# Optimization experiments

Measured on AMD Instinct MI355X. Metric: run time of the kernel, lower is better.

## Reference

```python
import jax, jax.numpy as jnp
import numpy as np

N_NODES = 50000
N_EDGES = 800000
IN_CH = 64
HID = 64
HID2 = HID // 2  # 32


def _sage_conv(x, src, dst, w_l, w_r, b, n_nodes):
    """PyG SAGEConv (aggr='mean', root_weight=True):
    out = lin_l(mean_{j in N(i)} x_j) + lin_r(x_i), bias in lin_l.
    Messages flow src -> dst (source_to_target)."""
    msg = x[src]  # [E, d] gather of source features
    summed = jax.ops.segment_sum(msg, dst, num_segments=n_nodes)  # [N, d]
    cnt = jax.ops.segment_sum(jnp.ones((src.shape[0],), x.dtype), dst,
                              num_segments=n_nodes)  # [N]
    mean = summed / jnp.maximum(cnt, 1.0)[:, None]
    return mean @ w_l + b + x @ w_r


def setup_inputs() -> dict:
    key = jax.random.key(0)
    ks = jax.random.split(key, 12)
    s = 0.05
    x = jax.random.normal(ks[0], (N_NODES, IN_CH), dtype=jnp.float32)
    edge_index = jax.random.randint(ks[1], (2, N_EDGES), 0, N_NODES, dtype=jnp.int32)
    return {
        "x": x,
        "edge_index": edge_index,
        # SAGEConv layer 1 (in -> hidden)
        "w1_l": jax.random.normal(ks[2], (IN_CH, HID), dtype=jnp.float32) * s,
        "w1_r": jax.random.normal(ks[3], (IN_CH, HID), dtype=jnp.float32) * s,
        "b1": jnp.zeros((HID,), jnp.float32),
        # SAGEConv layer 2 (hidden -> hidden//2)
        "w2_l": jax.random.normal(ks[4], (HID, HID2), dtype=jnp.float32) * s,
        "w2_r": jax.random.normal(ks[5], (HID, HID2), dtype=jnp.float32) * s,
        "b2": jnp.zeros((HID2,), jnp.float32),
        # classifier MLP: Linear(32,16) -> ReLU -> Linear(16,2)
        "wc1": jax.random.normal(ks[6], (HID2, 16), dtype=jnp.float32) * s,
        "bc1": jnp.zeros((16,), jnp.float32),
        "wc2": jax.random.normal(ks[7], (16, 2), dtype=jnp.float32) * s,
        "bc2": jnp.zeros((2,), jnp.float32),
    }


def reference(x, edge_index, w1_l, w1_r, b1, w2_l, w2_r, b2, wc1, bc1, wc2, bc2):
    src, dst = edge_index[0], edge_index[1]
    n = x.shape[0]
    # Dropout is identity in eval / deterministic reference.
    h = jax.nn.relu(_sage_conv(x, src, dst, w1_l, w1_r, b1, n))
    h = jax.nn.relu(_sage_conv(h, src, dst, w2_l, w2_r, b2, n))
    h = jax.nn.relu(h @ wc1 + bc1)
    out = h @ wc2 + bc2  # [N, 2]
    return out
```

## Files before the change

kernel.cpp:

```cpp
#include <hip/hip_runtime.h>
#include <hip/hip_fp16.h>

#define N_NODES 50000
#define N_EDGES 800000
#define NBINS   391
#define CAP     4096
#define EPB     4096
#define NBLK_E  ((N_EDGES + EPB - 1) / EPB)
#define NTILE   391
#define LSTRIDE 129

__global__ __launch_bounds__(512) void k_binA_pre1(
        const int* __restrict__ src, const int* __restrict__ dst,
        int* __restrict__ bincur, int* __restrict__ binned,
        const float* __restrict__ x,
        const float* __restrict__ wl, const float* __restrict__ wr,
        const float* __restrict__ b,
        __half* __restrict__ ph, float* __restrict__ q) {
    __shared__ float smem[64 * LSTRIDE];
    int t = threadIdx.x;
    int bb = blockIdx.x;
    if (bb < NBLK_E) {
        int* cnt  = (int*)smem;
        int* sc   = cnt + 392;
        int* lpos = sc + 512;
        int* base = lpos + 392;
        int* stage = base + 392;
        unsigned short* sbin = (unsigned short*)(stage + EPB);
        int blkbase = bb * EPB;
        int nE = min(EPB, N_EDGES - blkbase);
        for (int i = t; i < NBINS; i += 512) cnt[i] = 0;
        __syncthreads();
        int sv[8], dv[8];
#pragma unroll
        for (int k = 0; k < 8; ++k) {
            int e = blkbase + t + k * 512;
            if (e < N_EDGES) {
                sv[k] = src[e];
                dv[k] = dst[e];
                atomicAdd(&cnt[dv[k] >> 7], 1);
            } else dv[k] = -1;
        }
        __syncthreads();
        sc[t] = (t < NBINS) ? cnt[t] : 0;
        __syncthreads();
        for (int d = 1; d < 512; d <<= 1) {
            int add = (t >= d) ? sc[t - d] : 0;
            __syncthreads();
            sc[t] += add;
            __syncthreads();
        }
        for (int bi = t; bi < NBINS; bi += 512) {
            int excl = sc[bi] - cnt[bi];
            lpos[bi] = excl;
            sc[bi] = excl;
            if (cnt[bi] > 0) base[bi] = bi * CAP + atomicAdd(&bincur[bi], cnt[bi]);
        }
        __syncthreads();
#pragma unroll
        for (int k = 0; k < 8; ++k) {
            if (dv[k] >= 0) {
                int bi = dv[k] >> 7;
                int p = atomicAdd(&lpos[bi], 1);
                stage[p] = (sv[k] & 0xFFFF) | ((dv[k] & 127) << 16);
                sbin[p] = (unsigned short)bi;
            }
        }
        __syncthreads();
        for (int i = t; i < nE; i += 512) {
            int bi = sbin[i];
            int pos = base[bi] + (i - sc[bi]);
            if (pos < (bi + 1) * CAP) binned[pos] = stage[i];
        }
        return;
    }
    float* sx = smem;
    int g0 = (bb - NBLK_E) * 128;
#pragma unroll
    for (int i = 0; i < 4; ++i) {
        int f = t + i * 512;
        int nd = f >> 4, cq = f & 15;
        int gn = g0 + nd;
        float4 v = (gn < N_NODES) ? ((const float4*)x)[(size_t)gn * 16 + cq]
                                  : make_float4(0.f, 0.f, 0.f, 0.f);
        sx[(cq * 4 + 0) * LSTRIDE + nd] = v.x;
        sx[(cq * 4 + 1) * LSTRIDE + nd] = v.y;
        sx[(cq * 4 + 2) * LSTRIDE + nd] = v.z;
        sx[(cq * 4 + 3) * LSTRIDE + nd] = v.w;
    }
    __syncthreads();
    int role = __builtin_amdgcn_readfirstlane(t >> 7);
    int wsel = role >> 1;
    int c0 = (role & 1) * 32;
    int ln = t & 127;
    int node = g0 + ln;
    const float* __restrict__ wm = wsel ? wr : wl;
    float acc[32];
    if (wsel) {
#pragma unroll
        for (int c = 0; c < 32; ++c) acc[c] = b[c0 + c];
    } else {
#pragma unroll
        for (int c = 0; c < 32; ++c) acc[c] = 0.f;
    }
#pragma unroll
    for (int k = 0; k < 64; ++k) {
        float xk = sx[k * LSTRIDE + ln];
#pragma unroll
        for (int c = 0; c < 32; ++c)
            acc[c] = fmaf(xk, wm[k * 64 + c0 + c], acc[c]);
    }
    if (node >= N_NODES) return;
    if (wsel == 0) {
        alignas(16) __half2 hv[16];
#pragma unroll
        for (int i = 0; i < 16; ++i)
            hv[i] = __floats2half2_rn(acc[2 * i], acc[2 * i + 1]);
        float4* op = (float4*)(ph + (size_t)node * 64 + c0);
#pragma unroll
        for (int i = 0; i < 4; ++i) op[i] = ((float4*)hv)[i];
    } else {
        float4* op = (float4*)(q + (size_t)node * 64 + c0);
#pragma unroll
        for (int i = 0; i < 8; ++i)
            op[i] = make_float4(acc[4 * i], acc[4 * i + 1], acc[4 * i + 2], acc[4 * i + 3]);
    }
}

__global__ __launch_bounds__(512) void k_binB(const int* __restrict__ bincur,
                                              const int* __restrict__ binned,
                                              int* __restrict__ off,
                                              unsigned short* __restrict__ deg,
                                              int* __restrict__ esrc) {
    __shared__ int buf[CAP];
    __shared__ int cnt[128];
    __shared__ int tmp[128];
    __shared__ int cur[128];
    int bb = blockIdx.x, t = threadIdx.x;
    int n0 = bb << 7;
    int seg0 = bb * CAP;
    int n = min(bincur[bb], CAP);
    if (t < 128) cnt[t] = 0;
    __syncthreads();
    for (int i = t; i < n; i += 512) atomicAdd(&cnt[binned[seg0 + i] >> 16], 1);
    __syncthreads();
    int v = (t < 128) ? cnt[t] : 0;
    if (t < 128) tmp[t] = v;
    __syncthreads();
    int val = v;
    for (int d = 1; d < 128; d <<= 1) {
        int add = (t >= d && t < 128) ? tmp[t - d] : 0;
        __syncthreads();
        if (t < 128) { val += add; tmp[t] = val; }
        __syncthreads();
    }
    if (t < 128) {
        int excl = val - v;
        cur[t] = excl;
        int node = n0 + t;
        if (node < N_NODES) {
            off[node] = seg0 + excl;
            deg[node] = (unsigned short)v;
        }
    }
    __syncthreads();
    for (int i = t; i < n; i += 512) {
        int w = binned[seg0 + i];
        int p = atomicAdd(&cur[w >> 16], 1);
        buf[p] = w & 0xFFFF;
    }
    __syncthreads();
    for (int i = t; i < n; i += 512) esrc[seg0 + i] = buf[i];
}

__device__ __forceinline__ void add8(float2& c0, float2& c1, float2& c2, float2& c3,
                                     float4 rv) {
    const __half2* hp = (const __half2*)&rv;
    float2 f0 = __half22float2(hp[0]), f1 = __half22float2(hp[1]);
    float2 f2 = __half22float2(hp[2]), f3 = __half22float2(hp[3]);
    c0.x += f0.x; c0.y += f0.y; c1.x += f1.x; c1.y += f1.y;
    c2.x += f2.x; c2.y += f2.y; c3.x += f3.x; c3.y += f3.y;
}

#define RED2(v, M0, M1)                                         \
    v.x += __shfl_xor(v.x, M0); v.y += __shfl_xor(v.y, M0);     \
    v.x += __shfl_xor(v.x, M1); v.y += __shfl_xor(v.y, M1);

__global__ __launch_bounds__(1024) void k_agg1_pre2(
        const int* __restrict__ off, const unsigned short* __restrict__ deg,
        const int* __restrict__ esrc,
        const __half* __restrict__ ph, const float* __restrict__ q,
        const float* __restrict__ w2l, const float* __restrict__ w2r,
        const float* __restrict__ b2,
        __half* __restrict__ zh, float* __restrict__ r) {
    __shared__ float sx[64 * LSTRIDE];
    int t = threadIdx.x;
    int n0 = blockIdx.x << 7;
    int half = t >> 5;
    int l32 = t & 31;
    int eg = l32 >> 3;
    int cg = l32 & 7;
    for (int p = 0; p < 4; ++p) {
        int nl = half + 32 * p;
        int node = n0 + nl;
        if (node < N_NODES) {
            int s0 = off[node];
            int dv = deg[node];
            int s1 = s0 + dv;
            float2 A0 = make_float2(0.f, 0.f), A1 = A0, A2 = A0, A3 = A0;
            float2 B0 = A0, B1 = A0, B2 = A0, B3 = A0;
            for (int i = s0; i < s1; i += 8) {
                int i0 = i + eg, i1 = i + 4 + eg;
                if (i0 < s1) add8(A0, A1, A2, A3,
                    *(const float4*)(ph + (size_t)esrc[i0] * 64 + (cg << 3)));
                if (i1 < s1) add8(B0, B1, B2, B3,
                    *(const float4*)(ph + (size_t)esrc[i1] * 64 + (cg << 3)));
            }
            A0.x += B0.x; A0.y += B0.y; A1.x += B1.x; A1.y += B1.y;
            A2.x += B2.x; A2.y += B2.y; A3.x += B3.x; A3.y += B3.y;
            RED2(A0, 8, 16); RED2(A1, 8, 16); RED2(A2, 8, 16); RED2(A3, 8, 16);
            if (eg == 0) {
                float inv = 1.0f / fmaxf((float)dv, 1.0f);
                const float4* qp = (const float4*)(q + (size_t)node * 64 + (cg << 3));
                float4 q0 = qp[0], q1 = qp[1];
                float* d = sx + (cg << 3) * LSTRIDE + nl;
                d[0 * LSTRIDE] = fmaxf(fmaf(A0.x, inv, q0.x), 0.f);
                d[1 * LSTRIDE] = fmaxf(fmaf(A0.y, inv, q0.y), 0.f);
                d[2 * LSTRIDE] = fmaxf(fmaf(A1.x, inv, q0.z), 0.f);
                d[3 * LSTRIDE] = fmaxf(fmaf(A1.y, inv, q0.w), 0.f);
                d[4 * LSTRIDE] = fmaxf(fmaf(A2.x, inv, q1.x), 0.f);
                d[5 * LSTRIDE] = fmaxf(fmaf(A2.y, inv, q1.y), 0.f);
                d[6 * LSTRIDE] = fmaxf(fmaf(A3.x, inv, q1.z), 0.f);
                d[7 * LSTRIDE] = fmaxf(fmaf(A3.y, inv, q1.w), 0.f);
            }
        }
    }
    __syncthreads();
    int g = __builtin_amdgcn_readfirstlane(t >> 7);
    int role = g & 1;
    int c0 = (g >> 1) * 8;
    int ln = t & 127;
    int node = n0 + ln;
    const float* __restrict__ wm = role ? w2r : w2l;
    float acc[8];
    if (role) {
#pragma unroll
        for (int c = 0; c < 8; ++c) acc[c] = b2[c0 + c];
    } else {
#pragma unroll
        for (int c = 0; c < 8; ++c) acc[c] = 0.f;
    }
#pragma unroll
    for (int k = 0; k < 64; ++k) {
        float xk = sx[k * LSTRIDE + ln];
#pragma unroll
        for (int c = 0; c < 8; ++c)
            acc[c] = fmaf(xk, wm[k * 32 + c0 + c], acc[c]);
    }
    if (node >= N_NODES) return;
    if (role == 0) {
        alignas(16) __half2 hv[4];
#pragma unroll
        for (int i = 0; i < 4; ++i)
            hv[i] = __floats2half2_rn(acc[2 * i], acc[2 * i + 1]);
        *(float4*)(zh + (size_t)node * 32 + c0) = *(float4*)hv;
    } else {
        float4* op = (float4*)(r + (size_t)node * 32 + c0);
        op[0] = make_float4(acc[0], acc[1], acc[2], acc[3]);
        op[1] = make_float4(acc[4], acc[5], acc[6], acc[7]);
    }
}

__global__ __launch_bounds__(256) void k_agg2cls(const int* __restrict__ off,
                                                 const unsigned short* __restrict__ deg,
                                                 const int* __restrict__ esrc,
                                                 const __half* __restrict__ zh,
                                                 const float* __restrict__ r,
                                                 const float* __restrict__ wc1,
                                                 const float* __restrict__ bc1,
                                                 const float* __restrict__ wc2,
                                                 const float* __restrict__ bc2,
                                                 float* __restrict__ out) {
    __shared__ float sh2[16 * 33];
    __shared__ float sh3[16 * 17];
    __shared__ float swc1[512];
    __shared__ float sbc1[16];
    __shared__ float swc2[32];
    __shared__ float sbc2[2];
    int t = threadIdx.x;
    swc1[t] = wc1[t];
    swc1[t + 256] = wc1[t + 256];
    if (t < 16) sbc1[t] = bc1[t];
    if (t < 32) swc2[t] = wc2[t];
    if (t < 2)  sbc2[t] = bc2[t];

    int lane = t & 63;
    int l16 = lane & 15;
    int nl = (t >> 4) & 15;
    int node = blockIdx.x * 16 + nl;
    int eg = l16 >> 2;
    int cg = l16 & 3;
    int s0 = off[node];
    int dv = deg[node];
    int s1 = s0 + dv;
    float2 A0 = make_float2(0.f, 0.f), A1 = A0, A2 = A0, A3 = A0;
    float2 B0 = A0, B1 = A0, B2 = A0, B3 = A0;
    for (int i = s0; i < s1; i += 8) {
        int i0 = i + eg, i1 = i + 4 + eg;
        if (i0 < s1) add8(A0, A1, A2, A3,
            *(const float4*)(zh + (size_t)esrc[i0] * 32 + (cg << 3)));
        if (i1 < s1) add8(B0, B1, B2, B3,
            *(const float4*)(zh + (size_t)esrc[i1] * 32 + (cg << 3)));
    }
    A0.x += B0.x; A0.y += B0.y; A1.x += B1.x; A1.y += B1.y;
    A2.x += B2.x; A2.y += B2.y; A3.x += B3.x; A3.y += B3.y;
    RED2(A0, 4, 8); RED2(A1, 4, 8); RED2(A2, 4, 8); RED2(A3, 4, 8);
    if (eg == 0) {
        float inv = 1.0f / fmaxf((float)dv, 1.0f);
        const float4* rp = (const float4*)(r + (size_t)node * 32 + (cg << 3));
        float4 r0 = rp[0], r1 = rp[1];
        float* d = sh2 + nl * 33 + (cg << 3);
        d[0] = fmaxf(fmaf(A0.x, inv, r0.x), 0.f);
        d[1] = fmaxf(fmaf(A0.y, inv, r0.y), 0.f);
        d[2] = fmaxf(fmaf(A1.x, inv, r0.z), 0.f);
        d[3] = fmaxf(fmaf(A1.y, inv, r0.w), 0.f);
        d[4] = fmaxf(fmaf(A2.x, inv, r1.x), 0.f);
        d[5] = fmaxf(fmaf(A2.y, inv, r1.y), 0.f);
        d[6] = fmaxf(fmaf(A3.x, inv, r1.z), 0.f);
        d[7] = fmaxf(fmaf(A3.y, inv, r1.w), 0.f);
    }
    __syncthreads();
    int n = t >> 4, j = t & 15;
    float acc1 = sbc1[j];
#pragma unroll
    for (int k = 0; k < 32; ++k)
        acc1 = fmaf(sh2[n * 33 + k], swc1[k * 16 + j], acc1);
    sh3[n * 17 + j] = fmaxf(acc1, 0.f);
    __syncthreads();
    if (t < 16) {
        int nn = t;
        float o0 = sbc2[0], o1 = sbc2[1];
#pragma unroll
        for (int k = 0; k < 16; ++k) {
            float h3k = sh3[nn * 17 + k];
            o0 = fmaf(h3k, swc2[k * 2 + 0], o0);
            o1 = fmaf(h3k, swc2[k * 2 + 1], o1);
        }
        int gnode = blockIdx.x * 16 + nn;
        *(float2*)(out + (size_t)gnode * 2) = make_float2(o0, o1);
    }
}

extern "C" void kernel_launch(void* const* d_in, const int* in_sizes, int n_in,
                              void* d_out, int out_size, void* d_ws, size_t ws_size,
                              hipStream_t stream) {
    const float* x   = (const float*)d_in[0];
    const int*   ei  = (const int*)d_in[1];
    const int*   src = ei;
    const int*   dst = ei + N_EDGES;
    const float* w1l = (const float*)d_in[2];
    const float* w1r = (const float*)d_in[3];
    const float* b1  = (const float*)d_in[4];
    const float* w2l = (const float*)d_in[5];
    const float* w2r = (const float*)d_in[6];
    const float* b2  = (const float*)d_in[7];
    const float* wc1 = (const float*)d_in[8];
    const float* bc1 = (const float*)d_in[9];
    const float* wc2 = (const float*)d_in[10];
    const float* bc2 = (const float*)d_in[11];
    float* out = (float*)d_out;

    int*   wi     = (int*)d_ws;
    int*   bincur = wi;
    int*   binned = wi + 400;
    int*   esrc   = binned + (size_t)NBINS * CAP;
    int*   off    = esrc + (size_t)NBINS * CAP;
    unsigned short* deg = (unsigned short*)(off + N_NODES);
    float* q      = (float*)(deg + N_NODES + (N_NODES & 1));
    float* phf    = q + (size_t)64 * N_NODES;
    __half* ph    = (__half*)phf;
    float* zhf    = phf + (size_t)32 * N_NODES;
    __half* zh    = (__half*)zhf;
    float* r      = zhf + (size_t)16 * N_NODES;

    hipMemsetAsync(bincur, 0, 400 * sizeof(int), stream);
    k_binA_pre1<<<NBLK_E + NTILE, 512, 0, stream>>>(src, dst, bincur, binned,
                                                    x, w1l, w1r, b1, ph, q);
    k_binB<<<NBINS, 512, 0, stream>>>(bincur, binned, off, deg, esrc);
    k_agg1_pre2<<<NBINS, 1024, 0, stream>>>(off, deg, esrc, ph, q,
                                            w2l, w2r, b2, zh, r);
    k_agg2cls<<<N_NODES / 16, 256, 0, stream>>>(off, deg, esrc, zh, r,
                                                wc1, bc1, wc2, bc2, out);
}
```

Measured before the change: 181.5 us.

## Fuse per-bin counting sort into the layer-1 aggregation kernel

Merges the per-bin sort kernel into the first aggregation kernel, so each block sorts its bin's edges in shared memory and aggregates straight from the LDS copy of the sorted source indices and offsets. This removes one kernel launch and a global round trip for esrc/off/deg before aggregation, while still writing them out for the second layer. In exchange, LDS use per block grows (pool aliasing plus a 16KB index buffer), which may reduce occupancy, and the aggregation now waits behind the sort inside each block.

```diff
diff --git a/kernel.cpp b/kernel.cpp
--- a/kernel.cpp
+++ b/kernel.cpp
@@ -127,52 +127,6 @@
     }
 }
 
-__global__ __launch_bounds__(512) void k_binB(const int* __restrict__ bincur,
-                                              const int* __restrict__ binned,
-                                              int* __restrict__ off,
-                                              unsigned short* __restrict__ deg,
-                                              int* __restrict__ esrc) {
-    __shared__ int buf[CAP];
-    __shared__ int cnt[128];
-    __shared__ int tmp[128];
-    __shared__ int cur[128];
-    int bb = blockIdx.x, t = threadIdx.x;
-    int n0 = bb << 7;
-    int seg0 = bb * CAP;
-    int n = min(bincur[bb], CAP);
-    if (t < 128) cnt[t] = 0;
-    __syncthreads();
-    for (int i = t; i < n; i += 512) atomicAdd(&cnt[binned[seg0 + i] >> 16], 1);
-    __syncthreads();
-    int v = (t < 128) ? cnt[t] : 0;
-    if (t < 128) tmp[t] = v;
-    __syncthreads();
-    int val = v;
-    for (int d = 1; d < 128; d <<= 1) {
-        int add = (t >= d && t < 128) ? tmp[t - d] : 0;
-        __syncthreads();
-        if (t < 128) { val += add; tmp[t] = val; }
-        __syncthreads();
-    }
-    if (t < 128) {
-        int excl = val - v;
-        cur[t] = excl;
-        int node = n0 + t;
-        if (node < N_NODES) {
-            off[node] = seg0 + excl;
-            deg[node] = (unsigned short)v;
-        }
-    }
-    __syncthreads();
-    for (int i = t; i < n; i += 512) {
-        int w = binned[seg0 + i];
-        int p = atomicAdd(&cur[w >> 16], 1);
-        buf[p] = w & 0xFFFF;
-    }
-    __syncthreads();
-    for (int i = t; i < n; i += 512) esrc[seg0 + i] = buf[i];
-}
-
 __device__ __forceinline__ void add8(float2& c0, float2& c1, float2& c2, float2& c3,
                                      float4 rv) {
     const __half2* hp = (const __half2*)&rv;
@@ -186,16 +140,62 @@
     v.x += __shfl_xor(v.x, M0); v.y += __shfl_xor(v.y, M0);     \
     v.x += __shfl_xor(v.x, M1); v.y += __shfl_xor(v.y, M1);
 
-__global__ __launch_bounds__(1024) void k_agg1_pre2(
-        const int* __restrict__ off, const unsigned short* __restrict__ deg,
-        const int* __restrict__ esrc,
+__global__ __launch_bounds__(1024) void k_sort_agg1_pre2(
+        const int* __restrict__ bincur, const int* __restrict__ binned,
+        int* __restrict__ off, unsigned short* __restrict__ deg,
+        int* __restrict__ esrc,
         const __half* __restrict__ ph, const float* __restrict__ q,
         const float* __restrict__ w2l, const float* __restrict__ w2r,
         const float* __restrict__ b2,
         __half* __restrict__ zh, float* __restrict__ r) {
-    __shared__ float sx[64 * LSTRIDE];
+    __shared__ float poolA[64 * LSTRIDE];
+    __shared__ int   sbuf[CAP];
+    __shared__ int   loff[128];
+    __shared__ int   ldeg[128];
     int t = threadIdx.x;
-    int n0 = blockIdx.x << 7;
+    int bb = blockIdx.x;
+    int n0 = bb << 7;
+    int seg0 = bb * CAP;
+    int n = min(bincur[bb], CAP);
+    int* wbuf = (int*)poolA;
+    int* cnt  = wbuf + CAP;
+    int* tmp  = cnt + 128;
+    int* cur  = tmp + 128;
+    if (t < 128) cnt[t] = 0;
+    for (int i = t; i < n; i += 1024) wbuf[i] = binned[seg0 + i];
+    __syncthreads();
+    for (int i = t; i < n; i += 1024) atomicAdd(&cnt[wbuf[i] >> 16], 1);
+    __syncthreads();
+    int v = (t < 128) ? cnt[t] : 0;
+    if (t < 128) tmp[t] = v;
+    __syncthreads();
+    int val = v;
+    for (int d = 1; d < 128; d <<= 1) {
+        int add = (t >= d && t < 128) ? tmp[t - d] : 0;
+        __syncthreads();
+        if (t < 128) { val += add; tmp[t] = val; }
+        __syncthreads();
+    }
+    if (t < 128) {
+        int excl = val - v;
+        cur[t] = excl;
+        loff[t] = excl;
+        ldeg[t] = v;
+        int node = n0 + t;
+        if (node < N_NODES) {
+            off[node] = seg0 + excl;
+            deg[node] = (unsigned short)v;
+        }
+    }
+    __syncthreads();
+    for (int i = t; i < n; i += 1024) {
+        int w = wbuf[i];
+        int p = atomicAdd(&cur[w >> 16], 1);
+        sbuf[p] = w & 0xFFFF;
+    }
+    __syncthreads();
+    for (int i = t; i < n; i += 1024) esrc[seg0 + i] = sbuf[i];
+    float* sx = poolA;
     int half = t >> 5;
     int l32 = t & 31;
     int eg = l32 >> 3;
@@ -204,17 +204,17 @@
         int nl = half + 32 * p;
         int node = n0 + nl;
         if (node < N_NODES) {
-            int s0 = off[node];
-            int dv = deg[node];
+            int s0 = loff[nl];
+            int dv = ldeg[nl];
             int s1 = s0 + dv;
             float2 A0 = make_float2(0.f, 0.f), A1 = A0, A2 = A0, A3 = A0;
             float2 B0 = A0, B1 = A0, B2 = A0, B3 = A0;
             for (int i = s0; i < s1; i += 8) {
                 int i0 = i + eg, i1 = i + 4 + eg;
                 if (i0 < s1) add8(A0, A1, A2, A3,
-                    *(const float4*)(ph + (size_t)esrc[i0] * 64 + (cg << 3)));
+                    *(const float4*)(ph + (size_t)sbuf[i0] * 64 + (cg << 3)));
                 if (i1 < s1) add8(B0, B1, B2, B3,
-                    *(const float4*)(ph + (size_t)esrc[i1] * 64 + (cg << 3)));
+                    *(const float4*)(ph + (size_t)sbuf[i1] * 64 + (cg << 3)));
             }
             A0.x += B0.x; A0.y += B0.y; A1.x += B1.x; A1.y += B1.y;
             A2.x += B2.x; A2.y += B2.y; A3.x += B3.x; A3.y += B3.y;
@@ -386,9 +386,8 @@
     hipMemsetAsync(bincur, 0, 400 * sizeof(int), stream);
     k_binA_pre1<<<NBLK_E + NTILE, 512, 0, stream>>>(src, dst, bincur, binned,
                                                     x, w1l, w1r, b1, ph, q);
-    k_binB<<<NBINS, 512, 0, stream>>>(bincur, binned, off, deg, esrc);
-    k_agg1_pre2<<<NBINS, 1024, 0, stream>>>(off, deg, esrc, ph, q,
-                                            w2l, w2r, b2, zh, r);
+    k_sort_agg1_pre2<<<NBINS, 1024, 0, stream>>>(bincur, binned, off, deg, esrc,
+                                                 ph, q, w2l, w2r, b2, zh, r);
     k_agg2cls<<<N_NODES / 16, 256, 0, stream>>>(off, deg, esrc, zh, r,
                                                 wc1, bc1, wc2, bc2, out);
 }
```

Result: faster. 170.6 us (-6.0%).
